# Performance work log

Hardware: AMD Instinct MI355X
Metric: run time of the kernel (lower is better)

Reference implementation:

```python
import math
import jax, jax.numpy as jnp
import numpy as np

T, D, H = 2048, 1024, 16
DH = D // H
DFF = 4 * D
EPS = 1e-5


def gelu(x):
    c = math.sqrt(2.0 / math.pi)
    return 0.5 * x * (1.0 + jnp.tanh(c * (x + 0.044715 * jnp.power(x, 3))))


def layer_norm(x, w, b):
    mu = jnp.mean(x, axis=-1, keepdims=True)
    var = jnp.var(x, axis=-1, keepdims=True)
    return (x - mu) / jnp.sqrt(var + EPS) * w + b


def setup_inputs() -> dict:
    key = jax.random.key(0)
    ks = jax.random.split(key, 8)
    s = lambda fan_in: 1.0 / math.sqrt(fan_in)
    return {
        "x": jax.random.normal(ks[0], (T, D), jnp.float32),
        "w_kqv": jax.random.uniform(ks[1], (3 * D, D), jnp.float32, -s(D), s(D)),
        "b_kqv": jnp.zeros((3 * D,), jnp.float32),
        "w_o": jax.random.uniform(ks[2], (D, D), jnp.float32, -s(D), s(D)),
        "b_o": jnp.zeros((D,), jnp.float32),
        "ln1_w": jnp.ones((D,), jnp.float32),
        "ln1_b": jnp.zeros((D,), jnp.float32),
        "ln2_w": jnp.ones((D,), jnp.float32),
        "ln2_b": jnp.zeros((D,), jnp.float32),
        "w_up": jax.random.uniform(ks[3], (DFF, D), jnp.float32, -s(D), s(D)),
        "b_up": jnp.zeros((DFF,), jnp.float32),
        "w_down": jax.random.uniform(ks[4], (D, DFF), jnp.float32, -s(DFF), s(DFF)),
        "b_down": jnp.zeros((D,), jnp.float32),
    }


def _block(x, w_kqv, b_kqv, w_o, b_o, ln1_w, ln1_b, ln2_w, ln2_b,
           w_up, b_up, w_down, b_down):
    t = x.shape[0]
    # --- causal attention ---
    h = layer_norm(x, ln1_w, ln1_b)
    kqv = h @ w_kqv.T + b_kqv                      # [t, 3D]
    k, q, v = jnp.split(kqv, 3, axis=-1)
    # rearrange 't (d h) -> h t d' : head index is the FAST axis (as in source)
    to_heads = lambda m: m.reshape(t, DH, H).transpose(2, 0, 1)  # [H, t, DH]
    k, q, v = to_heads(k), to_heads(q), to_heads(v)
    # NOTE: source divides by sqrt(1/d) == multiplies by sqrt(d_head)
    logits = jnp.einsum('hqd,hkd->hqk', q, k) * math.sqrt(DH)
    mask = jnp.tril(jnp.ones((t, t), dtype=bool))
    logits = jnp.where(mask, logits, -jnp.inf)
    attn_w = jax.nn.softmax(logits, axis=-1)       # [H, t, t]
    hv = jnp.einsum('hqK,hKd->hqd', attn_w, v)     # [H, t, DH]
    # rearrange 'h q d -> q (h d)' : head index is the SLOW axis (as in source)
    hv = hv.transpose(1, 0, 2).reshape(t, D)
    x = x + (hv @ w_o.T + b_o)
    # --- MLP ---
    h2 = layer_norm(x, ln2_w, ln2_b)
    z = gelu(h2 @ w_up.T + b_up) @ w_down.T + b_down
    return x + z


def reference(x, w_kqv, b_kqv, w_o, b_o, ln1_w, ln1_b, ln2_w, ln2_b,
              w_up, b_up, w_down, b_down):
    return _block(x, w_kqv, b_kqv, w_o, b_o, ln1_w, ln1_b, ln2_w, ln2_b,
                  w_up, b_up, w_down, b_down)
```

## Files before the change

### kernel.cpp

```cpp
#include <hip/hip_runtime.h>
#include <math.h>

#define TT 2048
#define DD 1024
#define NH 16
#define DHD 64
#define DFF 4096

typedef __attribute__((ext_vector_type(8))) short short8;
typedef __attribute__((ext_vector_type(4))) float f32x4;

#define MFMA16(a, b, c) __builtin_amdgcn_mfma_f32_16x16x32_bf16(a, b, c, 0, 0, 0)
#define GLDS16(gp, lp) __builtin_amdgcn_global_load_lds( \
    (const __attribute__((address_space(1))) void*)(gp), \
    (__attribute__((address_space(3))) void*)(lp), 16, 0, 0)

static __device__ __forceinline__ unsigned short f2b(float f) {
  unsigned u = __builtin_bit_cast(unsigned, f);
  u = u + 0x7fffu + ((u >> 16) & 1u);
  return (unsigned short)(u >> 16);
}
static __device__ __forceinline__ float b2f(unsigned short b) {
  return __builtin_bit_cast(float, (unsigned)b << 16);
}

__global__ __launch_bounds__(256) void f2b4_kernel(const float* __restrict__ s0,
    const float* __restrict__ s1, const float* __restrict__ s2,
    const float* __restrict__ s3, unsigned short* __restrict__ out) {
  int i = blockIdx.x * 256 + threadIdx.x;
  float4 v;
  if (i < 786432) {
    int row = i >> 8, kk = i & 255;
    int sec = row >> 10, wi = row & 1023;
    int src = (sec << 10) + ((wi & 63) << 4) + (wi >> 6);
    v = ((const float4*)s0)[(src << 8) + kk];
  } else if (i < 1048576) {
    v = ((const float4*)s1)[i - 786432];
  } else if (i < 2097152) {
    v = ((const float4*)s2)[i - 1048576];
  } else {
    v = ((const float4*)s3)[i - 2097152];
  }
  ushort4 o;
  o.x = f2b(v.x); o.y = f2b(v.y); o.z = f2b(v.z); o.w = f2b(v.w);
  ((ushort4*)out)[i] = o;
}

__global__ __launch_bounds__(256) void ln_kernel(const float* __restrict__ x,
    const float* __restrict__ w, const float* __restrict__ b,
    unsigned short* __restrict__ out) {
  int row = blockIdx.x;
  const float4* xr = (const float4*)(x + (size_t)row * DD);
  float4 v = xr[threadIdx.x];
  float s  = v.x + v.y + v.z + v.w;
  float ss = v.x * v.x + v.y * v.y + v.z * v.z + v.w * v.w;
  for (int o = 32; o > 0; o >>= 1) {
    s  += __shfl_down(s, o);
    ss += __shfl_down(ss, o);
  }
  __shared__ float red[10];
  int lane = threadIdx.x & 63, wv = threadIdx.x >> 6;
  if (lane == 0) { red[wv] = s; red[4 + wv] = ss; }
  __syncthreads();
  if (threadIdx.x == 0) {
    float S  = red[0] + red[1] + red[2] + red[3];
    float SS = red[4] + red[5] + red[6] + red[7];
    float mu  = S * (1.0f / DD);
    float var = SS * (1.0f / DD) - mu * mu;
    red[8] = mu;
    red[9] = rsqrtf(var + 1e-5f);
  }
  __syncthreads();
  float mu = red[8], inv = red[9];
  float4 wv4 = ((const float4*)w)[threadIdx.x];
  float4 bv4 = ((const float4*)b)[threadIdx.x];
  ushort4 o4;
  o4.x = f2b((v.x - mu) * inv * wv4.x + bv4.x);
  o4.y = f2b((v.y - mu) * inv * wv4.y + bv4.y);
  o4.z = f2b((v.z - mu) * inv * wv4.z + bv4.z);
  o4.w = f2b((v.w - mu) * inv * wv4.w + bv4.w);
  ((ushort4*)(out + (size_t)row * DD))[threadIdx.x] = o4;
}

__global__ __launch_bounds__(256, 4) void gemm6(
    const unsigned short* __restrict__ A,
    const unsigned short* __restrict__ Bw,
    unsigned short* __restrict__ Cp,
    unsigned short* __restrict__ Cp2,
    int M, int N, int K, int KS, int CX, int CY, int SPLITA) {
  __shared__ char lds[32768];
  const int tid = threadIdx.x;
  const int w = tid >> 6, l = tid & 63;
  const int l15 = l & 15, lhi = l >> 4;

  const int GX = N >> 7, GYM = M >> 7;
  const int xcd = blockIdx.x & 7, s = blockIdx.x >> 3;
  const int ncx = GX / CX;
  const int bx = (xcd % ncx) * CX + (s % CX);
  const int yz = (xcd / ncx) * CY + (s / CX);
  const int by = yz % GYM, bz = yz / GYM;

  const int row0 = by << 7, col0 = bx << 7;
  const int kbeg = bz * KS;
  const int wm = (w >> 1) * 64, wn = (w & 1) * 64;

  f32x4 acc[4][4] = {};

  const int srow = w * 32 + (l >> 2);
  const int scol = (l & 3) * 16;
  const char* aS = (const char*)A + ((size_t)(row0 + srow) * K + kbeg) * 2 + scol;
  const char* bS = (const char*)Bw + ((size_t)(col0 + srow) * K + kbeg) * 2 + scol;
  const size_t r16 = (size_t)K * 32;
  const int aO = w * 2048, bO = 8192 + w * 2048;
  const int NT = KS >> 5;

  auto STAGE = [&](int t) {
    char* base = lds + (t & 1) * 16384;
    const char* a = aS + (size_t)t * 64;
    const char* b = bS + (size_t)t * 64;
    GLDS16(a,       base + aO);
    GLDS16(a + r16, base + aO + 1024);
    GLDS16(b,       base + bO);
    GLDS16(b + r16, base + bO + 1024);
  };
  auto COMPUTE = [&](int t) {
    const char* Ab = lds + (t & 1) * 16384;
    const char* Bb = Ab + 8192;
    short8 af[4], bf[4];
#pragma unroll
    for (int mi = 0; mi < 4; ++mi)
      af[mi] = *(const short8*)(Ab + (wm + mi * 16 + l15) * 64 + lhi * 16);
#pragma unroll
    for (int ni = 0; ni < 4; ++ni)
      bf[ni] = *(const short8*)(Bb + (wn + ni * 16 + l15) * 64 + lhi * 16);
    __builtin_amdgcn_s_setprio(1);
#pragma unroll
    for (int mi = 0; mi < 4; ++mi)
#pragma unroll
      for (int ni = 0; ni < 4; ++ni)
        acc[mi][ni] = MFMA16(af[mi], bf[ni], acc[mi][ni]);
    __builtin_amdgcn_s_setprio(0);
  };

  STAGE(0);
  for (int t = 0; t < NT; ++t) {
    if (t + 1 < NT) STAGE(t + 1);
    __builtin_amdgcn_sched_barrier(0);
    if (t + 1 < NT) asm volatile("s_waitcnt vmcnt(4)" ::: "memory");
    else            asm volatile("s_waitcnt vmcnt(0)" ::: "memory");
    __builtin_amdgcn_s_barrier();
    __builtin_amdgcn_sched_barrier(0);
    COMPUTE(t);
    __builtin_amdgcn_sched_barrier(0);
    __builtin_amdgcn_s_barrier();
  }

  unsigned short* base;
  size_t off;
  if (bz < SPLITA) { base = Cp;  off = (size_t)bz * M * N; }
  else             { base = Cp2; off = (size_t)(bz - SPLITA) * M * N; }
#pragma unroll
  for (int mi = 0; mi < 4; ++mi)
#pragma unroll
    for (int r = 0; r < 4; ++r) {
      size_t row = (size_t)(row0 + wm + mi * 16 + lhi * 4 + r);
#pragma unroll
      for (int ni = 0; ni < 4; ++ni)
        base[off + row * N + col0 + wn + ni * 16 + l15] = f2b(acc[mi][ni][r]);
    }
}

template<int MODE>
__global__ __launch_bounds__(256) void reduce2b(const unsigned short* __restrict__ p0,
    const unsigned short* __restrict__ p1, const float* __restrict__ bias,
    unsigned short* __restrict__ out, int n4) {
  int i = blockIdx.x * 256 + threadIdx.x;
  ushort4 a = ((const ushort4*)p0)[i];
  ushort4 b = ((const ushort4*)p1)[i];
  float4 bb = ((const float4*)bias)[i % n4];
  float v0 = b2f(a.x) + b2f(b.x) + bb.x;
  float v1 = b2f(a.y) + b2f(b.y) + bb.y;
  float v2 = b2f(a.z) + b2f(b.z) + bb.z;
  float v3 = b2f(a.w) + b2f(b.w) + bb.w;
  if (MODE == 1) {
    const float c = 0.7978845608028654f;
    v0 = 0.5f * v0 * (1.0f + tanhf(c * (v0 + 0.044715f * v0 * v0 * v0)));
    v1 = 0.5f * v1 * (1.0f + tanhf(c * (v1 + 0.044715f * v1 * v1 * v1)));
    v2 = 0.5f * v2 * (1.0f + tanhf(c * (v2 + 0.044715f * v2 * v2 * v2)));
    v3 = 0.5f * v3 * (1.0f + tanhf(c * (v3 + 0.044715f * v3 * v3 * v3)));
  }
  if (MODE == 2) {
    int c4 = i % 768;
    if (c4 >= 256 && c4 < 512) { v0 *= 8.f; v1 *= 8.f; v2 *= 8.f; v3 *= 8.f; }
  }
  ushort4 o;
  o.x = f2b(v0); o.y = f2b(v1); o.z = f2b(v2); o.w = f2b(v3);
  ((ushort4*)out)[i] = o;
}

__global__ __launch_bounds__(256) void reduce4_ln(const unsigned short* __restrict__ p,
    const float* __restrict__ bias, const float* __restrict__ resid,
    const float* __restrict__ lnw, const float* __restrict__ lnb,
    float* __restrict__ x2, unsigned short* __restrict__ hout) {
  int row = blockIdx.x;
  int i = row * 256 + threadIdx.x;
  float4 r = ((const float4*)resid)[i];
  float4 bb = ((const float4*)bias)[threadIdx.x];
  float o0 = r.x + bb.x, o1 = r.y + bb.y, o2 = r.z + bb.z, o3 = r.w + bb.w;
#pragma unroll
  for (int z = 0; z < 4; ++z) {
    ushort4 pv = ((const ushort4*)(p + (size_t)z * TT * DD))[i];
    o0 += b2f(pv.x); o1 += b2f(pv.y); o2 += b2f(pv.z); o3 += b2f(pv.w);
  }
  float4 o; o.x = o0; o.y = o1; o.z = o2; o.w = o3;
  ((float4*)x2)[i] = o;
  float s  = o0 + o1 + o2 + o3;
  float ss = o0 * o0 + o1 * o1 + o2 * o2 + o3 * o3;
  for (int of = 32; of > 0; of >>= 1) {
    s  += __shfl_down(s, of);
    ss += __shfl_down(ss, of);
  }
  __shared__ float red[10];
  int lane = threadIdx.x & 63, wv = threadIdx.x >> 6;
  if (lane == 0) { red[wv] = s; red[4 + wv] = ss; }
  __syncthreads();
  if (threadIdx.x == 0) {
    float S  = red[0] + red[1] + red[2] + red[3];
    float SS = red[4] + red[5] + red[6] + red[7];
    float mu  = S * (1.0f / DD);
    float var = SS * (1.0f / DD) - mu * mu;
    red[8] = mu;
    red[9] = rsqrtf(var + 1e-5f);
  }
  __syncthreads();
  float mu = red[8], inv = red[9];
  float4 wv4 = ((const float4*)lnw)[threadIdx.x];
  float4 bv4 = ((const float4*)lnb)[threadIdx.x];
  ushort4 o4;
  o4.x = f2b((o0 - mu) * inv * wv4.x + bv4.x);
  o4.y = f2b((o1 - mu) * inv * wv4.y + bv4.y);
  o4.z = f2b((o2 - mu) * inv * wv4.z + bv4.z);
  o4.w = f2b((o3 - mu) * inv * wv4.w + bv4.w);
  ((ushort4*)(hout + (size_t)row * DD))[threadIdx.x] = o4;
}

__global__ __launch_bounds__(256) void reduce8(const unsigned short* __restrict__ pA,
    const unsigned short* __restrict__ pB, const float* __restrict__ bias,
    const float* __restrict__ resid, float* __restrict__ out) {
  int i = blockIdx.x * 256 + threadIdx.x;
  float4 r = ((const float4*)resid)[i];
  float4 bb = ((const float4*)bias)[i & (DD / 4 - 1)];
  float o0 = r.x + bb.x, o1 = r.y + bb.y, o2 = r.z + bb.z, o3 = r.w + bb.w;
#pragma unroll
  for (int z = 0; z < 4; ++z) {
    ushort4 pv = ((const ushort4*)(pA + (size_t)z * TT * DD))[i];
    o0 += b2f(pv.x); o1 += b2f(pv.y); o2 += b2f(pv.z); o3 += b2f(pv.w);
    ushort4 qv = ((const ushort4*)(pB + (size_t)z * TT * DD))[i];
    o0 += b2f(qv.x); o1 += b2f(qv.y); o2 += b2f(qv.z); o3 += b2f(qv.w);
  }
  float4 o; o.x = o0; o.y = o1; o.z = o2; o.w = o3;
  ((float4*)out)[i] = o;
}

__global__ __launch_bounds__(256) void transpose_v(const unsigned short* __restrict__ kqz,
    unsigned short* __restrict__ Vt) {
  const int h = blockIdx.y;
  const int t0 = blockIdx.x * 64;
  __shared__ unsigned short Vs[64][65];
  for (int idx = threadIdx.x; idx < 4096; idx += 256) {
    int t = idx >> 6, d = idx & 63;
    Vs[t][d] = kqz[(size_t)(t0 + t) * (3 * DD) + 2 * DD + h * 64 + d];
  }
  __syncthreads();
  for (int idx = threadIdx.x; idx < 4096; idx += 256) {
    int d = idx >> 6, t = idx & 63;
    Vt[(size_t)(h * DHD + d) * TT + t0 + t] = Vs[t][d];
  }
}

__global__ __launch_bounds__(256) void attn4(
    const unsigned short* __restrict__ kqz,
    const unsigned short* __restrict__ Vt,
    unsigned short* __restrict__ hv) {
  const int bid = blockIdx.x;
  const int xcd = bid & 7, s = bid >> 3;
  const int hs = s >> 5, j = s & 31;
  const int qb = hs ? j : 31 - j;
  const int h  = xcd * 2 + hs;
  const int q0 = qb * 64;
  const int tid = threadIdx.x;
  const int w = tid >> 6, l = tid & 63;
  const int l15 = l & 15, lhi = l >> 4;

  __shared__ char lds[81920];
  char* Ps = lds + 65536 + w * 4096;

  const char* kqzB = (const char*)kqz;
  const char* VhB  = (const char*)(Vt + (size_t)h * DHD * TT);
  const size_t KROW = 3 * DD * 2;
  const size_t VROW = TT * 2;

  const unsigned short* Qb = kqz + (size_t)(q0 + w * 16 + l15) * (3 * DD) + DD + h * 64;
  short8 qf0 = *(const short8*)(Qb + lhi * 8);
  short8 qf1 = *(const short8*)(Qb + 32 + lhi * 8);

  f32x4 oacc[4] = {};
  float m = -1e30f, lsum = 0.0f;

  const int kr8 = l >> 3;
  const int kcolb = ((l & 7) * 16) ^ (kr8 << 4);
  const int vg = l >> 4;
  const int vbase = (l & 15) * 16;
  const int kswz = (l15 & 7) << 4;
  const int vpswz = (l15 & 15) << 4;

  auto stageKV = [&](int kt2) {
    const int buf = kt2 & 1;
    const int k0n = kt2 * 128;
    char* kb = lds + buf * 16384 + w * 4096;
    const char* ks = kqzB + (size_t)(k0n + w * 32 + kr8) * KROW + h * 128 + kcolb;
    GLDS16(ks,             kb);
    GLDS16(ks +  8 * KROW, kb + 1024);
    GLDS16(ks + 16 * KROW, kb + 2048);
    GLDS16(ks + 24 * KROW, kb + 3072);
    char* vb = lds + 32768 + buf * 16384 + w * 4096;
    const char* vs = VhB + (size_t)(w * 16 + vg) * VROW + (size_t)k0n * 2;
    GLDS16(vs +             (vbase ^ ((vg +  0) << 4)), vb);
    GLDS16(vs +  4 * VROW + (vbase ^ ((vg +  4) << 4)), vb + 1024);
    GLDS16(vs +  8 * VROW + (vbase ^ ((vg +  8) << 4)), vb + 2048);
    GLDS16(vs + 12 * VROW + (vbase ^ ((vg + 12) << 4)), vb + 3072);
  };

  const int NT = (qb + 2) >> 1;
  stageKV(0);
  if (NT > 1) stageKV(1);

  for (int kt = 0; kt < NT; ++kt) {
    const int k0 = kt * 128;
    __builtin_amdgcn_sched_barrier(0);
    if (kt + 1 < NT) asm volatile("s_waitcnt vmcnt(8)" ::: "memory");
    else             asm volatile("s_waitcnt vmcnt(0)" ::: "memory");
    __builtin_amdgcn_s_barrier();
    __builtin_amdgcn_sched_barrier(0);

    const char* Kb = lds + (kt & 1) * 16384;
    const char* Vb = lds + 32768 + (kt & 1) * 16384;

    f32x4 sacc[8] = {};
    __builtin_amdgcn_s_setprio(1);
#pragma unroll
    for (int nt = 0; nt < 8; ++nt) {
      const char* rp = Kb + (nt * 16 + l15) * 128;
      short8 kb0 = *(const short8*)(rp + ((lhi * 16) ^ kswz));
      short8 kb1 = *(const short8*)(rp + ((64 + lhi * 16) ^ kswz));
      sacc[nt] = MFMA16(kb0, qf0, sacc[nt]);
      sacc[nt] = MFMA16(kb1, qf1, sacc[nt]);
    }
    __builtin_amdgcn_s_setprio(0);

    if (kt == NT - 1) {
      const int qq = q0 + w * 16 + l15;
#pragma unroll
      for (int nt = 0; nt < 8; ++nt)
#pragma unroll
        for (int r = 0; r < 4; ++r)
          if (k0 + nt * 16 + lhi * 4 + r > qq) sacc[nt][r] = -1e30f;
    }

    float tmax = -1e30f;
#pragma unroll
    for (int nt = 0; nt < 8; ++nt)
#pragma unroll
      for (int r = 0; r < 4; ++r) tmax = fmaxf(tmax, sacc[nt][r]);
    tmax = fmaxf(tmax, __shfl_xor(tmax, 16));
    tmax = fmaxf(tmax, __shfl_xor(tmax, 32));
    float mnew = fmaxf(m, tmax);
    float al = __expf(m - mnew);
    m = mnew;
    float ssum = 0.0f;
#pragma unroll
    for (int nt = 0; nt < 8; ++nt)
#pragma unroll
      for (int r = 0; r < 4; ++r) {
        float p = __expf(sacc[nt][r] - mnew);
        sacc[nt][r] = p;
        ssum += p;
      }
    ssum += __shfl_xor(ssum, 16);
    ssum += __shfl_xor(ssum, 32);
    lsum = lsum * al + ssum;

    {
      char* pp = Ps + l15 * 256;
#pragma unroll
      for (int nt = 0; nt < 8; ++nt) {
        uint2 pk;
        pk.x = (unsigned)f2b(sacc[nt][0]) | ((unsigned)f2b(sacc[nt][1]) << 16);
        pk.y = (unsigned)f2b(sacc[nt][2]) | ((unsigned)f2b(sacc[nt][3]) << 16);
        *(uint2*)(pp + ((nt * 32 + lhi * 8) ^ vpswz)) = pk;
      }
    }

    float alr[4];
#pragma unroll
    for (int r = 0; r < 4; ++r) alr[r] = __shfl(al, (l & 48) | (lhi * 4 + r));
#pragma unroll
    for (int dt = 0; dt < 4; ++dt)
#pragma unroll
      for (int r = 0; r < 4; ++r) oacc[dt][r] *= alr[r];

    const char* pr = Ps + l15 * 256;
    short8 pa[4];
#pragma unroll
    for (int kc = 0; kc < 4; ++kc)
      pa[kc] = *(const short8*)(pr + ((kc * 64 + lhi * 16) ^ vpswz));
    __builtin_amdgcn_s_setprio(1);
#pragma unroll
    for (int dt = 0; dt < 4; ++dt) {
      const char* vr = Vb + (dt * 16 + l15) * 256;
#pragma unroll
      for (int kc = 0; kc < 4; ++kc) {
        short8 vbf = *(const short8*)(vr + ((kc * 64 + lhi * 16) ^ vpswz));
        oacc[dt] = MFMA16(pa[kc], vbf, oacc[dt]);
      }
    }
    __builtin_amdgcn_s_setprio(0);

    __builtin_amdgcn_sched_barrier(0);
    __builtin_amdgcn_s_barrier();
    if (kt + 2 < NT) stageKV(kt + 2);
  }

  float lr4[4];
#pragma unroll
  for (int r = 0; r < 4; ++r)
    lr4[r] = 1.0f / __shfl(lsum, (l & 48) | (lhi * 4 + r));
#pragma unroll
  for (int r = 0; r < 4; ++r) {
    size_t orow = (size_t)(q0 + w * 16 + lhi * 4 + r) * DD + h * 64;
#pragma unroll
    for (int dt = 0; dt < 4; ++dt)
      hv[orow + dt * 16 + l15] = f2b(oacc[dt][r] * lr4[r]);
  }
}

extern "C" void kernel_launch(void* const* d_in, const int* in_sizes, int n_in,
                              void* d_out, int out_size, void* d_ws, size_t ws_size,
                              hipStream_t stream) {
  const float* x     = (const float*)d_in[0];
  const float* w_kqv = (const float*)d_in[1];
  const float* b_kqv = (const float*)d_in[2];
  const float* w_o   = (const float*)d_in[3];
  const float* b_o   = (const float*)d_in[4];
  const float* ln1_w = (const float*)d_in[5];
  const float* ln1_b = (const float*)d_in[6];
  const float* ln2_w = (const float*)d_in[7];
  const float* ln2_b = (const float*)d_in[8];
  const float* w_up  = (const float*)d_in[9];
  const float* b_up  = (const float*)d_in[10];
  const float* w_dn  = (const float*)d_in[11];
  const float* b_dn  = (const float*)d_in[12];
  float* out = (float*)d_out;

  char* W = (char*)d_ws;
  unsigned short* wkqv_b = (unsigned short*)(W);
  unsigned short* wo_b   = (unsigned short*)(W + 6291456);
  unsigned short* wup_b  = (unsigned short*)(W + 8388608);
  unsigned short* wdn_b  = (unsigned short*)(W + 16777216);
  unsigned short* h_b    = (unsigned short*)(W + 25165824);
  unsigned short* rA     = (unsigned short*)(W + 29360128);
  unsigned short* rB     = (unsigned short*)(W + 46137344);
  unsigned short* Vtg    = (unsigned short*)(W + 54525952);
  unsigned short* hv_b   = (unsigned short*)(W + 58720256);
  float*          x2     = (float*)(W + 62914560);
  unsigned short* pB2    = (unsigned short*)(W);

  f2b4_kernel<<<3145728 / 256, 256, 0, stream>>>(w_kqv, w_o, w_up, w_dn, wkqv_b);

  ln_kernel<<<TT, 256, 0, stream>>>(x, ln1_w, ln1_b, h_b);
  gemm6<<<768, 256, 0, stream>>>(h_b, wkqv_b, rA, rB,
      TT, 3 * DD, DD, DD / 2, 3, 32, 1);
  reduce2b<2><<<TT * 3 * DD / 4 / 256, 256, 0, stream>>>(
      rA, rB, b_kqv, rA, 3 * DD / 4);
  transpose_v<<<dim3(TT / 64, NH), 256, 0, stream>>>(rA, Vtg);
  attn4<<<512, 256, 0, stream>>>(rA, Vtg, hv_b);
  gemm6<<<512, 256, 0, stream>>>(hv_b, wo_b, rA, rA,
      TT, DD, DD, DD / 4, 1, 64, 4);
  reduce4_ln<<<TT, 256, 0, stream>>>(rA, b_o, x, ln2_w, ln2_b, x2, h_b);
  gemm6<<<1024, 256, 0, stream>>>(h_b, wup_b, rA, rB,
      TT, DFF, DD, DD / 2, 4, 32, 1);
  reduce2b<1><<<TT * DFF / 4 / 256, 256, 0, stream>>>(
      rA, rB, b_up, rA, DFF / 4);
  gemm6<<<1024, 256, 0, stream>>>(rA, wdn_b, rB, pB2,
      TT, DD, DFF, DFF / 8, 1, 128, 4);
  reduce8<<<TT * DD / 4 / 256, 256, 0, stream>>>(rB, pB2, b_dn, x2, out);
}
```

Before: 184.3 us.

## Split attention KV range across two blocks and merge partial softmax results

Each (head, query-block) attention tile is split into two blocks that each process half of the causal key tiles. Each writes normalized partial outputs plus its running max and sum, and a new merge kernel combines the two halves with log-sum-exp weights. This doubles the grid to improve load balance and occupancy for the long causal rows. The cost is an extra kernel launch, extra global traffic for the partial outputs, and an added bf16 rounding step. The block ordering also changes from interleaved heavy/light query blocks to descending query-block order.

```diff
diff --git a/kernel.cpp b/kernel.cpp
--- a/kernel.cpp
+++ b/kernel.cpp
@@ -278,19 +278,40 @@
   }
 }
 
-__global__ __launch_bounds__(256) void attn4(
+__global__ __launch_bounds__(256) void attn5(
     const unsigned short* __restrict__ kqz,
     const unsigned short* __restrict__ Vt,
-    unsigned short* __restrict__ hv) {
+    unsigned short* __restrict__ hvp,
+    float2* __restrict__ mlarr) {
   const int bid = blockIdx.x;
   const int xcd = bid & 7, s = bid >> 3;
-  const int hs = s >> 5, j = s & 31;
-  const int qb = hs ? j : 31 - j;
+  const int half = s & 1;
+  const int j = s >> 1;
+  const int hs = j & 1;
+  const int qb = 31 - (j >> 1);
   const int h  = xcd * 2 + hs;
   const int q0 = qb * 64;
+  const int NT = (qb + 2) >> 1;
+  const int t0 = half ? (NT + 1) >> 1 : 0;
+  const int t1 = half ? NT : (NT + 1) >> 1;
+
   const int tid = threadIdx.x;
   const int w = tid >> 6, l = tid & 63;
   const int l15 = l & 15, lhi = l >> 4;
+
+  unsigned short* hvO = hvp + (size_t)half * TT * DD;
+  float2* mlO = mlarr + (size_t)(half * NH + h) * TT;
+
+  if (t0 >= t1) {
+#pragma unroll
+    for (int r = 0; r < 4; ++r) {
+      size_t orow = (size_t)(q0 + w * 16 + lhi * 4 + r) * DD + h * 64;
+#pragma unroll
+      for (int dt = 0; dt < 4; ++dt) hvO[orow + dt * 16 + l15] = 0;
+    }
+    if (lhi == 0) mlO[q0 + w * 16 + l15] = make_float2(-1e30f, 0.0f);
+    return;
+  }
 
   __shared__ char lds[81920];
   char* Ps = lds + 65536 + w * 4096;
@@ -331,14 +352,13 @@
     GLDS16(vs + 12 * VROW + (vbase ^ ((vg + 12) << 4)), vb + 3072);
   };
 
-  const int NT = (qb + 2) >> 1;
-  stageKV(0);
-  if (NT > 1) stageKV(1);
-
-  for (int kt = 0; kt < NT; ++kt) {
+  stageKV(t0);
+  if (t0 + 1 < t1) stageKV(t0 + 1);
+
+  for (int kt = t0; kt < t1; ++kt) {
     const int k0 = kt * 128;
     __builtin_amdgcn_sched_barrier(0);
-    if (kt + 1 < NT) asm volatile("s_waitcnt vmcnt(8)" ::: "memory");
+    if (kt + 1 < t1) asm volatile("s_waitcnt vmcnt(8)" ::: "memory");
     else             asm volatile("s_waitcnt vmcnt(0)" ::: "memory");
     __builtin_amdgcn_s_barrier();
     __builtin_amdgcn_sched_barrier(0);
@@ -428,20 +448,47 @@
 
     __builtin_amdgcn_sched_barrier(0);
     __builtin_amdgcn_s_barrier();
-    if (kt + 2 < NT) stageKV(kt + 2);
+    if (kt + 2 < t1) stageKV(kt + 2);
   }
 
   float lr4[4];
 #pragma unroll
-  for (int r = 0; r < 4; ++r)
-    lr4[r] = 1.0f / __shfl(lsum, (l & 48) | (lhi * 4 + r));
+  for (int r = 0; r < 4; ++r) {
+    float lv = __shfl(lsum, (l & 48) | (lhi * 4 + r));
+    lr4[r] = 1.0f / lv;
+  }
 #pragma unroll
   for (int r = 0; r < 4; ++r) {
     size_t orow = (size_t)(q0 + w * 16 + lhi * 4 + r) * DD + h * 64;
 #pragma unroll
     for (int dt = 0; dt < 4; ++dt)
-      hv[orow + dt * 16 + l15] = f2b(oacc[dt][r] * lr4[r]);
-  }
+      hvO[orow + dt * 16 + l15] = f2b(oacc[dt][r] * lr4[r]);
+  }
+  if (lhi == 0) mlO[q0 + w * 16 + l15] = make_float2(m, lsum);
+}
+
+__global__ __launch_bounds__(256) void merge_attn(
+    const unsigned short* __restrict__ hvp, const float2* __restrict__ mlarr,
+    unsigned short* __restrict__ hv) {
+  int row = blockIdx.x;
+  int t = threadIdx.x;
+  int h = t >> 4;
+  float2 ml0 = mlarr[(size_t)h * TT + row];
+  float2 ml1 = mlarr[(size_t)(NH + h) * TT + row];
+  float M = fmaxf(ml0.x, ml1.x);
+  float w0 = ml0.y * __expf(ml0.x - M);
+  float w1 = ml1.y * __expf(ml1.x - M);
+  float inv = 1.0f / (w0 + w1);
+  w0 *= inv; w1 *= inv;
+  size_t i = (size_t)row * 256 + t;
+  ushort4 a = ((const ushort4*)hvp)[i];
+  ushort4 b = ((const ushort4*)(hvp + (size_t)TT * DD))[i];
+  ushort4 o;
+  o.x = f2b(w0 * b2f(a.x) + w1 * b2f(b.x));
+  o.y = f2b(w0 * b2f(a.y) + w1 * b2f(b.y));
+  o.z = f2b(w0 * b2f(a.z) + w1 * b2f(b.z));
+  o.w = f2b(w0 * b2f(a.w) + w1 * b2f(b.w));
+  ((ushort4*)hv)[i] = o;
 }
 
 extern "C" void kernel_launch(void* const* d_in, const int* in_sizes, int n_in,
@@ -468,8 +515,10 @@
   unsigned short* wup_b  = (unsigned short*)(W + 8388608);
   unsigned short* wdn_b  = (unsigned short*)(W + 16777216);
   unsigned short* h_b    = (unsigned short*)(W + 25165824);
+  float2*         mlarr  = (float2*)(W + 25165824);
   unsigned short* rA     = (unsigned short*)(W + 29360128);
   unsigned short* rB     = (unsigned short*)(W + 46137344);
+  unsigned short* hvhalf = (unsigned short*)(W + 46137344);
   unsigned short* Vtg    = (unsigned short*)(W + 54525952);
   unsigned short* hv_b   = (unsigned short*)(W + 58720256);
   float*          x2     = (float*)(W + 62914560);
@@ -483,7 +532,8 @@
   reduce2b<2><<<TT * 3 * DD / 4 / 256, 256, 0, stream>>>(
       rA, rB, b_kqv, rA, 3 * DD / 4);
   transpose_v<<<dim3(TT / 64, NH), 256, 0, stream>>>(rA, Vtg);
-  attn4<<<512, 256, 0, stream>>>(rA, Vtg, hv_b);
+  attn5<<<1024, 256, 0, stream>>>(rA, Vtg, hvhalf, mlarr);
+  merge_attn<<<TT, 256, 0, stream>>>(hvhalf, mlarr, hv_b);
   gemm6<<<512, 256, 0, stream>>>(hv_b, wo_b, rA, rA,
       TT, DD, DD, DD / 4, 1, 64, 4);
   reduce4_ln<<<TT, 256, 0, stream>>>(rA, b_o, x, ln2_w, ln2_b, x2, h_b);
```

Measured after the change: 186.7 us. Within noise of the previous version (+1.3%).
